# Optimization experiments

Hardware: AMD Instinct MI355X
Metric: run time of the kernel (lower is better)

## Reference

```python
import jax, jax.numpy as jnp
import numpy as np

D = 1024
E = 8


def setup_inputs() -> dict:
    key = jax.random.key(0)
    ks = jax.random.split(key, 7)
    s = 1.0 / np.sqrt(D)
    x = jax.random.normal(ks[0], (4, 2048, D), dtype=jnp.float32)
    Wg = jax.random.uniform(ks[1], (D, E), minval=-s, maxval=s, dtype=jnp.float32)
    bg = jax.random.uniform(ks[2], (E,), minval=-s, maxval=s, dtype=jnp.float32)
    W1 = jax.random.uniform(ks[3], (E, D, D), minval=-s, maxval=s, dtype=jnp.float32)
    b1 = jax.random.uniform(ks[4], (E, D), minval=-s, maxval=s, dtype=jnp.float32)
    W2 = jax.random.uniform(ks[5], (E, D, D), minval=-s, maxval=s, dtype=jnp.float32)
    b2 = jax.random.uniform(ks[6], (E, D), minval=-s, maxval=s, dtype=jnp.float32)
    return {"x": x, "Wg": Wg, "bg": bg, "W1": W1, "b1": b1, "W2": W2, "b2": b2}


def reference(x, Wg, bg, W1, b1, W2, b2):
    N, T, d = x.shape
    x_flat = x.reshape(N * T, d)                                  # [NT, D]
    logits = x_flat @ Wg + bg                                     # [NT, E]
    probs = jax.nn.softmax(logits, axis=-1)
    assignments = jnp.argmax(probs, axis=-1)                      # [NT]
    # all-experts MLP (dense, as in the original module)
    h = jnp.einsum('nd,edh->neh', x_flat, W1) + b1[None]          # [NT, E, D]
    h = jax.nn.gelu(h, approximate=False)                         # torch GELU = exact erf
    eo = jnp.einsum('neh,ehd->ned', h, W2) + b2[None]             # [NT, E, D]
    selected = jnp.take_along_axis(eo, assignments[:, None, None], axis=1)[:, 0, :]  # [NT, D]
    w = jnp.take_along_axis(probs, assignments[:, None], axis=1)  # [NT, 1]
    out = (w * selected).reshape(N, T, d)
    return out
```

## Files before the change

kernel.cpp:

```cpp
#include <hip/hip_runtime.h>
#include <cstdint>

#define NT 8192
#define DD 1024
#define NE 8
#define BK 32
#define NKIT (DD / BK)
#define TM 64
#define MAXTILE 136

typedef __attribute__((ext_vector_type(8))) _Float16 half8;
typedef __attribute__((ext_vector_type(4))) float f32x4;

__device__ __forceinline__ unsigned short f2h_bits(float f) {
  _Float16 h = (_Float16)f;
  return __builtin_bit_cast(unsigned short, h);
}

#define GLDS16(gp, lp) __builtin_amdgcn_global_load_lds( \
  (__attribute__((address_space(1))) void*)(uintptr_t)(gp), \
  (__attribute__((address_space(3))) void*)(uintptr_t)(lp), 16, 0, 0)

#define WAITCNT_VM3  0xF73
#define WAITCNT_VM0  0xF70

__global__ __launch_bounds__(256) void wcast_kernel(
    const float* __restrict__ W1, const float* __restrict__ W2,
    _Float16* __restrict__ W1t, _Float16* __restrict__ W2t) {
  __shared__ float tile[64][65];
  const int z = blockIdx.z;
  const float* W = (z < 8 ? W1 : W2) + (size_t)(z & 7) * (DD * DD);
  _Float16* Wt   = (z < 8 ? W1t : W2t) + (size_t)(z & 7) * (DD * DD);
  const int k0 = blockIdx.x * 64, n0 = blockIdx.y * 64;
  const int tid = threadIdx.x;
#pragma unroll
  for (int it = 0; it < 4; ++it) {
    int idx = it * 256 + tid;
    int r = idx >> 4;
    int q = idx & 15;
    float4 v = *(const float4*)(W + (size_t)(k0 + r) * DD + n0 + q * 4);
    tile[r][q * 4 + 0] = v.x; tile[r][q * 4 + 1] = v.y;
    tile[r][q * 4 + 2] = v.z; tile[r][q * 4 + 3] = v.w;
  }
  __syncthreads();
#pragma unroll
  for (int it = 0; it < 4; ++it) {
    int idx = it * 256 + tid;
    int n = idx >> 4;
    int q = idx & 15;
    ushort4 o;
    o.x = f2h_bits(tile[q * 4 + 0][n]);
    o.y = f2h_bits(tile[q * 4 + 1][n]);
    o.z = f2h_bits(tile[q * 4 + 2][n]);
    o.w = f2h_bits(tile[q * 4 + 3][n]);
    *(ushort4*)(Wt + (size_t)(n0 + n) * DD + k0 + q * 4) = o;
  }
}

__global__ __launch_bounds__(256) void gate_kernel(
    const float* __restrict__ x, const float* __restrict__ Wg, const float* __restrict__ bg,
    int* __restrict__ assign, float* __restrict__ wgt, _Float16* __restrict__ xh) {
  __shared__ float WgL[NE * DD];
  const int tid = threadIdx.x;
#pragma unroll
  for (int it = 0; it < 8; ++it) {
    int idx = it * 256 + tid;
    float4 v = ((const float4*)Wg)[idx];
    int k = idx >> 1;
    int e0 = (idx & 1) * 4;
    WgL[(e0 + 0) * DD + k] = v.x;
    WgL[(e0 + 1) * DD + k] = v.y;
    WgL[(e0 + 2) * DD + k] = v.z;
    WgL[(e0 + 3) * DD + k] = v.w;
  }
  __syncthreads();
  const int lane = tid & 63, w = tid >> 6;
#pragma unroll
  for (int s = 0; s < 2; ++s) {
    const int t = blockIdx.x * 8 + w * 2 + s;
    const float4* xr = (const float4*)(x + (size_t)t * DD);
    float4 xv[4];
#pragma unroll
    for (int c = 0; c < 4; ++c) xv[c] = xr[lane + 64 * c];
    ushort4* xo = (ushort4*)(xh + (size_t)t * DD);
#pragma unroll
    for (int c = 0; c < 4; ++c) {
      union { ushort4 u; _Float16 h[4]; } cv;
      cv.h[0] = (_Float16)xv[c].x; cv.h[1] = (_Float16)xv[c].y;
      cv.h[2] = (_Float16)xv[c].z; cv.h[3] = (_Float16)xv[c].w;
      xo[lane + 64 * c] = cv.u;
    }
    float p[NE];
#pragma unroll
    for (int e = 0; e < NE; ++e) {
      float acc = 0.f;
#pragma unroll
      for (int c = 0; c < 4; ++c) {
        float4 wv = *(const float4*)&WgL[e * DD + 4 * lane + 256 * c];
        acc += xv[c].x * wv.x + xv[c].y * wv.y + xv[c].z * wv.z + xv[c].w * wv.w;
      }
      p[e] = acc;
    }
#pragma unroll
    for (int e = 0; e < NE; ++e) {
      float v = p[e];
      for (int off = 32; off > 0; off >>= 1) v += __shfl_down(v, off, 64);
      p[e] = v;
    }
    if (lane == 0) {
      float l[NE];
#pragma unroll
      for (int e = 0; e < NE; ++e) l[e] = p[e] + bg[e];
      int a = 0; float best = l[0];
#pragma unroll
      for (int e = 1; e < NE; ++e) if (l[e] > best) { best = l[e]; a = e; }
      float sum = 0.f;
#pragma unroll
      for (int e = 0; e < NE; ++e) sum += expf(l[e] - best);
      assign[t] = a;
      wgt[t] = 1.0f / sum;
    }
  }
}

__global__ __launch_bounds__(1024) void sort_kernel(
    const int* __restrict__ assign, int* __restrict__ rowtok, int* __restrict__ plan) {
  __shared__ int sc[NE * 1024];
  const int tid = threadIdx.x;
  int a[8];
  int c[NE];
#pragma unroll
  for (int e = 0; e < NE; ++e) c[e] = 0;
#pragma unroll
  for (int j = 0; j < 8; ++j) { a[j] = assign[tid * 8 + j]; ++c[a[j]]; }
#pragma unroll
  for (int e = 0; e < NE; ++e) sc[e * 1024 + tid] = c[e];
  __syncthreads();
  for (int d = 1; d < 1024; d <<= 1) {
    int add[NE];
    if (tid >= d) {
#pragma unroll
      for (int e = 0; e < NE; ++e) add[e] = sc[e * 1024 + tid - d];
    }
    __syncthreads();
    if (tid >= d) {
#pragma unroll
      for (int e = 0; e < NE; ++e) sc[e * 1024 + tid] += add[e];
    }
    __syncthreads();
  }
  int tot[NE], incl[NE];
#pragma unroll
  for (int e = 0; e < NE; ++e) { tot[e] = sc[e * 1024 + 1023]; incl[e] = sc[e * 1024 + tid]; }
  int offs[NE];
  {
    int s = 0;
#pragma unroll
    for (int e = 0; e < NE; ++e) { offs[e] = s; s += tot[e]; }
  }
  int run[NE];
#pragma unroll
  for (int e = 0; e < NE; ++e) run[e] = offs[e] + incl[e] - c[e];
#pragma unroll
  for (int j = 0; j < 8; ++j) { int e = a[j]; rowtok[run[e]++] = tid * 8 + j; }
  if (tid == 0) {
    int nt = 0;
    for (int e = 0; e < NE; ++e) {
      int cc = tot[e], st = offs[e];
      int t_cnt = (cc + TM - 1) / TM;
      for (int t = 0; t < t_cnt; ++t) {
        plan[1 + nt] = e;
        plan[1 + MAXTILE + nt] = st + t * TM;
        plan[1 + 2 * MAXTILE + nt] = st + cc;
        ++nt;
      }
    }
    plan[0] = nt;
  }
}

template <int MODE>
__global__ __launch_bounds__(256) void gemm_kernel(
    const _Float16* __restrict__ A,
    const _Float16* __restrict__ Wt,
    const float* __restrict__ bias,
    const int* __restrict__ plan,
    _Float16* __restrict__ Hout,
    float* __restrict__ Fout,
    const int* __restrict__ rowtok,
    const float* __restrict__ wgt) {
  const int wrk = blockIdx.x;
  const int tile = wrk >> 3;
  if (tile >= plan[0]) return;
  const int e = plan[1 + tile];
  const int m0 = plan[1 + MAXTILE + tile];
  const int seg_end = plan[1 + 2 * MAXTILE + tile];
  const int n0 = (wrk & 7) * 128;

  const int tid = threadIdx.x;
  const int lane = tid & 63;
  const int wn = tid >> 6;
  const int quad = lane >> 4;
  const int r15 = lane & 15;

  __shared__ alignas(16) char lds[24576];
  char* ldsA = lds;
  char* ldsB = lds + 8192;

  const _Float16* We = Wt + (size_t)e * DD * DD;
  const _Float16* gAp;
  const _Float16* gBp[2];
  int ldsoA, ldsoB[2];
  {
    int slot = tid;
    int row = slot >> 2;
    int c = (slot & 3) ^ ((row >> 1) & 3);
    int rg = m0 + row; if (rg > NT - 1) rg = NT - 1;
    int arow = (MODE == 0) ? rowtok[rg] : rg;
    gAp = A + (size_t)arow * DD + c * 8;
    ldsoA = slot * 16;
  }
#pragma unroll
  for (int i = 0; i < 2; ++i) {
    int slot = i * 256 + tid;
    int row = slot >> 2;
    int c = (slot & 3) ^ ((row >> 1) & 3);
    gBp[i] = We + (size_t)(n0 + row) * DD + c * 8;
    ldsoB[i] = slot * 16;
  }

  int aoff[4], boff[2];
#pragma unroll
  for (int i = 0; i < 4; ++i) {
    int m = i * 16 + r15;
    aoff[i] = m * 4 + (quad ^ ((m >> 1) & 3));
  }
#pragma unroll
  for (int i = 0; i < 2; ++i) {
    int n = wn * 32 + i * 16 + r15;
    boff[i] = n * 4 + (quad ^ ((n >> 1) & 3));
  }

  f32x4 acc[4][2];
  f32x4 zero4 = {0.f, 0.f, 0.f, 0.f};
#pragma unroll
  for (int mi = 0; mi < 4; ++mi)
#pragma unroll
    for (int ni = 0; ni < 2; ++ni) acc[mi][ni] = zero4;

#define STAGE(KT, BUF) do {                                          \
    const int ko_ = (KT) * BK;                                       \
    char* la_ = ldsA + ((BUF) << 12);                                \
    char* lb_ = ldsB + ((BUF) << 13);                                \
    GLDS16(gAp + ko_, la_ + ldsoA);                                  \
    GLDS16(gBp[0] + ko_, lb_ + ldsoB[0]);                            \
    GLDS16(gBp[1] + ko_, lb_ + ldsoB[1]);                            \
  } while (0)

  STAGE(0, 0);

#pragma unroll 1
  for (int kt = 0; kt < NKIT; ++kt) {
    const int buf = kt & 1;
    __builtin_amdgcn_s_barrier();
    __asm__ volatile("" ::: "memory");
    if (kt + 1 < NKIT) {
      STAGE(kt + 1, buf ^ 1);
      __builtin_amdgcn_s_waitcnt(WAITCNT_VM3);
    } else {
      __builtin_amdgcn_s_waitcnt(WAITCNT_VM0);
    }
    __builtin_amdgcn_s_barrier();
    __asm__ volatile("" ::: "memory");
    const half8* AsV = (const half8*)(ldsA + (buf << 12));
    const half8* BsV = (const half8*)(ldsB + (buf << 13));
    half8 a[4], b[2];
#pragma unroll
    for (int i = 0; i < 4; ++i) a[i] = AsV[aoff[i]];
#pragma unroll
    for (int i = 0; i < 2; ++i) b[i] = BsV[boff[i]];
#pragma unroll
    for (int mi = 0; mi < 4; ++mi)
#pragma unroll
      for (int ni = 0; ni < 2; ++ni)
        acc[mi][ni] = __builtin_amdgcn_mfma_f32_16x16x32_f16(a[mi], b[ni], acc[mi][ni], 0, 0, 0);
  }
#undef STAGE

  const float* bptr = bias + (size_t)e * DD;
#pragma unroll
  for (int mi = 0; mi < 4; ++mi) {
    int rowb = m0 + mi * 16 + quad * 4;
#pragma unroll
    for (int r = 0; r < 4; ++r) {
      int gpos = rowb + r;
      if (gpos < seg_end) {
        if (MODE == 0) {
#pragma unroll
          for (int ni = 0; ni < 2; ++ni) {
            int n = n0 + wn * 32 + ni * 16 + r15;
            float val = acc[mi][ni][r] + bptr[n];
            val = 0.5f * val * (1.0f + erff(val * 0.70710678118654752f));
            Hout[(size_t)gpos * DD + n] = (_Float16)val;
          }
        } else {
          int tok = rowtok[gpos];
          float wv = wgt[tok];
          float* orow = Fout + (size_t)tok * DD;
#pragma unroll
          for (int ni = 0; ni < 2; ++ni) {
            int n = n0 + wn * 32 + ni * 16 + r15;
            orow[n] = (acc[mi][ni][r] + bptr[n]) * wv;
          }
        }
      }
    }
  }
}

extern "C" void kernel_launch(void* const* d_in, const int* in_sizes, int n_in,
                              void* d_out, int out_size, void* d_ws, size_t ws_size,
                              hipStream_t stream) {
  const float* x  = (const float*)d_in[0];
  const float* Wg = (const float*)d_in[1];
  const float* bg = (const float*)d_in[2];
  const float* W1 = (const float*)d_in[3];
  const float* b1 = (const float*)d_in[4];
  const float* W2 = (const float*)d_in[5];
  const float* b2 = (const float*)d_in[6];
  float* out = (float*)d_out;

  char* ws = (char*)d_ws;
  const size_t MB16 = (size_t)1 << 24;
  _Float16* W1t = (_Float16*)(ws + 0 * MB16);
  _Float16* W2t = (_Float16*)(ws + 1 * MB16);
  _Float16* xh  = (_Float16*)(ws + 2 * MB16);
  _Float16* H   = (_Float16*)(ws + 3 * MB16);
  int*   assign = (int*)(ws + 4 * MB16);
  int*   rowtok = assign + NT;
  float* wgt    = (float*)(rowtok + NT);
  int*   plan   = (int*)(wgt + NT);

  wcast_kernel<<<dim3(16, 16, 16), 256, 0, stream>>>(W1, W2, W1t, W2t);
  gate_kernel<<<NT / 8, 256, 0, stream>>>(x, Wg, bg, assign, wgt, xh);
  sort_kernel<<<1, 1024, 0, stream>>>(assign, rowtok, plan);
  gemm_kernel<0><<<MAXTILE * 8, 256, 0, stream>>>(xh, W1t, b1, plan, H, nullptr, rowtok, nullptr);
  gemm_kernel<1><<<MAXTILE * 8, 256, 0, stream>>>(H, W2t, b2, plan, nullptr, out, rowtok, wgt);
}
```

Before: 254.0 us.

## Deepen GEMM LDS pipeline to four stages with one barrier per k-step

The grouped expert GEMM moves from a double-buffered LDS scheme with two barriers per k-iteration to a four-buffer ring. Three tiles are prefetched ahead and a single waitcnt plus barrier guards each step, which hides more global-load latency and removes one barrier per iteration. LDS use grows from 24KB to 48KB per block, which may lower occupancy. The sort kernel's serial single-thread tile-plan construction is also replaced by a parallel fill in which each thread writes one plan entry.

```diff
diff --git a/kernel.cpp b/kernel.cpp
--- a/kernel.cpp
+++ b/kernel.cpp
@@ -21,6 +21,7 @@
   (__attribute__((address_space(1))) void*)(uintptr_t)(gp), \
   (__attribute__((address_space(3))) void*)(uintptr_t)(lp), 16, 0, 0)
 
+#define WAITCNT_VM6  0xF76
 #define WAITCNT_VM3  0xF73
 #define WAITCNT_VM0  0xF70
 
@@ -126,6 +127,7 @@
 __global__ __launch_bounds__(1024) void sort_kernel(
     const int* __restrict__ assign, int* __restrict__ rowtok, int* __restrict__ plan) {
   __shared__ int sc[NE * 1024];
+  __shared__ int s_pref[NE + 1];
   const int tid = threadIdx.x;
   int a[8];
   int c[NE];
@@ -164,18 +166,20 @@
 #pragma unroll
   for (int j = 0; j < 8; ++j) { int e = a[j]; rowtok[run[e]++] = tid * 8 + j; }
   if (tid == 0) {
-    int nt = 0;
-    for (int e = 0; e < NE; ++e) {
-      int cc = tot[e], st = offs[e];
-      int t_cnt = (cc + TM - 1) / TM;
-      for (int t = 0; t < t_cnt; ++t) {
-        plan[1 + nt] = e;
-        plan[1 + MAXTILE + nt] = st + t * TM;
-        plan[1 + 2 * MAXTILE + nt] = st + cc;
-        ++nt;
-      }
-    }
-    plan[0] = nt;
+    int s = 0;
+    for (int e = 0; e < NE; ++e) { s_pref[e] = s; s += (tot[e] + TM - 1) / TM; }
+    s_pref[NE] = s;
+    plan[0] = s;
+  }
+  __syncthreads();
+  const int nt = s_pref[NE];
+  if (tid < nt) {
+    int e = 0;
+    while (tid >= s_pref[e + 1]) ++e;
+    int t = tid - s_pref[e];
+    plan[1 + tid] = e;
+    plan[1 + MAXTILE + tid] = offs[e] + t * TM;
+    plan[1 + 2 * MAXTILE + tid] = offs[e] + tot[e];
   }
 }
 
@@ -203,9 +207,7 @@
   const int quad = lane >> 4;
   const int r15 = lane & 15;
 
-  __shared__ alignas(16) char lds[24576];
-  char* ldsA = lds;
-  char* ldsB = lds + 8192;
+  __shared__ alignas(16) char lds[49152];
 
   const _Float16* We = Wt + (size_t)e * DD * DD;
   const _Float16* gAp;
@@ -248,44 +250,56 @@
 #pragma unroll
     for (int ni = 0; ni < 2; ++ni) acc[mi][ni] = zero4;
 
+#define LDSBUF(B) (lds + (B) * 12288)
 #define STAGE(KT, BUF) do {                                          \
     const int ko_ = (KT) * BK;                                       \
-    char* la_ = ldsA + ((BUF) << 12);                                \
-    char* lb_ = ldsB + ((BUF) << 13);                                \
-    GLDS16(gAp + ko_, la_ + ldsoA);                                  \
-    GLDS16(gBp[0] + ko_, lb_ + ldsoB[0]);                            \
-    GLDS16(gBp[1] + ko_, lb_ + ldsoB[1]);                            \
+    char* lb_ = LDSBUF(BUF);                                         \
+    GLDS16(gAp + ko_, lb_ + ldsoA);                                  \
+    GLDS16(gBp[0] + ko_, lb_ + 4096 + ldsoB[0]);                     \
+    GLDS16(gBp[1] + ko_, lb_ + 4096 + ldsoB[1]);                     \
   } while (0)
+#define COMPUTE(BUF) do {                                            \
+    const half8* AsV = (const half8*)(LDSBUF(BUF));                  \
+    const half8* BsV = (const half8*)(LDSBUF(BUF) + 4096);           \
+    half8 a_[4], b_[2];                                              \
+    _Pragma("unroll")                                                \
+    for (int i = 0; i < 4; ++i) a_[i] = AsV[aoff[i]];                \
+    _Pragma("unroll")                                                \
+    for (int i = 0; i < 2; ++i) b_[i] = BsV[boff[i]];                \
+    _Pragma("unroll")                                                \
+    for (int mi = 0; mi < 4; ++mi)                                   \
+      _Pragma("unroll")                                              \
+      for (int ni = 0; ni < 2; ++ni)                                 \
+        acc[mi][ni] = __builtin_amdgcn_mfma_f32_16x16x32_f16(a_[mi], b_[ni], acc[mi][ni], 0, 0, 0); \
+  } while (0)
 
   STAGE(0, 0);
+  STAGE(1, 1);
+  STAGE(2, 2);
 
 #pragma unroll 1
-  for (int kt = 0; kt < NKIT; ++kt) {
-    const int buf = kt & 1;
+  for (int kt = 0; kt < NKIT - 3; ++kt) {
+    __builtin_amdgcn_s_waitcnt(WAITCNT_VM6);
     __builtin_amdgcn_s_barrier();
     __asm__ volatile("" ::: "memory");
-    if (kt + 1 < NKIT) {
-      STAGE(kt + 1, buf ^ 1);
-      __builtin_amdgcn_s_waitcnt(WAITCNT_VM3);
-    } else {
-      __builtin_amdgcn_s_waitcnt(WAITCNT_VM0);
-    }
-    __builtin_amdgcn_s_barrier();
-    __asm__ volatile("" ::: "memory");
-    const half8* AsV = (const half8*)(ldsA + (buf << 12));
-    const half8* BsV = (const half8*)(ldsB + (buf << 13));
-    half8 a[4], b[2];
-#pragma unroll
-    for (int i = 0; i < 4; ++i) a[i] = AsV[aoff[i]];
-#pragma unroll
-    for (int i = 0; i < 2; ++i) b[i] = BsV[boff[i]];
-#pragma unroll
-    for (int mi = 0; mi < 4; ++mi)
-#pragma unroll
-      for (int ni = 0; ni < 2; ++ni)
-        acc[mi][ni] = __builtin_amdgcn_mfma_f32_16x16x32_f16(a[mi], b[ni], acc[mi][ni], 0, 0, 0);
-  }
+    STAGE(kt + 3, (kt + 3) & 3);
+    COMPUTE(kt & 3);
+  }
+  __builtin_amdgcn_s_waitcnt(WAITCNT_VM6);
+  __builtin_amdgcn_s_barrier();
+  __asm__ volatile("" ::: "memory");
+  COMPUTE((NKIT - 3) & 3);
+  __builtin_amdgcn_s_waitcnt(WAITCNT_VM3);
+  __builtin_amdgcn_s_barrier();
+  __asm__ volatile("" ::: "memory");
+  COMPUTE((NKIT - 2) & 3);
+  __builtin_amdgcn_s_waitcnt(WAITCNT_VM0);
+  __builtin_amdgcn_s_barrier();
+  __asm__ volatile("" ::: "memory");
+  COMPUTE((NKIT - 1) & 3);
+#undef COMPUTE
 #undef STAGE
+#undef LDSBUF
 
   const float* bptr = bias + (size_t)e * DD;
 #pragma unroll
```

Result: no change. 255.9 us (+0.7%).
